# Kernel optimization log

Measured on AMD Instinct MI355X. Metric: run time of the kernel, lower is better.

The kernel has to match this reference:

```python
import jax, jax.numpy as jnp
import numpy as np

B, S, D, H, DFF, L, VOCAB = 4, 2048, 512, 8, 2048, 6, 32000
DK = D // H


def positional_encoding(n_step, d):
    pos = jnp.arange(n_step, dtype=jnp.float32)[:, None]            # (S,1)
    i = jnp.arange(d, dtype=jnp.float32)                            # (D,)
    ang = pos * (1.0 / jnp.power(10000.0, 2.0 * jnp.floor(i / 2.0) / d))
    odd = (jnp.arange(d) % 2).astype(bool)
    return jnp.where(odd, jnp.cos(ang), jnp.sin(ang))               # (S,D)


def layer_norm(x, g, b, eps=1e-6):
    m = x.mean(-1, keepdims=True)
    v = ((x - m) ** 2).mean(-1, keepdims=True)
    return g * (x - m) * jax.lax.rsqrt(v + eps) + b


def mha(Q, K, V, Wq, bq, Wo, bo, mask):
    # Faithful to source: Wq is (buggily) used for Q, K and V projections.
    def split(t):
        return t.reshape(t.shape[0], -1, H, DK).transpose(0, 2, 1, 3)  # (B,H,S,dk)
    q = split(Q @ Wq + bq)
    k = split(K @ Wq + bq)
    v = split(V @ Wq + bq)
    scores = jnp.einsum('bhqd,bhkd->bhqk', q, k) / jnp.sqrt(jnp.float32(DK))
    if mask is not None:
        scores = scores + mask * (-1e9)
    attn = jax.nn.softmax(scores, axis=-1)
    out = jnp.einsum('bhqk,bhkd->bhqd', attn, v)
    out = out.transpose(0, 2, 1, 3).reshape(Q.shape[0], -1, D)
    return out @ Wo + bo


def setup_inputs() -> dict:
    key = jax.random.key(0)
    ks = jax.random.split(key, 16)
    inputs = jax.random.randint(ks[0], (B, S), 0, VOCAB)
    enc_inputs = jax.random.normal(ks[1], (B, S, D), dtype=jnp.float32)
    # causal mask (1 = masked) broadcast over heads, per source mask*-1e9 convention
    comb = 1.0 - jnp.tril(jnp.ones((S, S), dtype=jnp.float32))
    comb_mask = jnp.broadcast_to(comb, (B, 1, S, S))
    padding_mask = jnp.zeros((B, 1, 1, S), dtype=jnp.float32)
    s = 0.02
    emb = jax.random.normal(ks[2], (VOCAB, D), dtype=jnp.float32) * s
    Wq1 = jax.random.normal(ks[3], (L, D, D), dtype=jnp.float32) * s
    bq1 = jnp.zeros((L, D), dtype=jnp.float32)
    Wo1 = jax.random.normal(ks[4], (L, D, D), dtype=jnp.float32) * s
    bo1 = jnp.zeros((L, D), dtype=jnp.float32)
    Wq2 = jax.random.normal(ks[5], (L, D, D), dtype=jnp.float32) * s
    bq2 = jnp.zeros((L, D), dtype=jnp.float32)
    Wo2 = jax.random.normal(ks[6], (L, D, D), dtype=jnp.float32) * s
    bo2 = jnp.zeros((L, D), dtype=jnp.float32)
    W1 = jax.random.normal(ks[7], (L, D, DFF), dtype=jnp.float32) * s
    b1 = jnp.zeros((L, DFF), dtype=jnp.float32)
    W2 = jax.random.normal(ks[8], (L, DFF, D), dtype=jnp.float32) * s
    b2 = jnp.zeros((L, D), dtype=jnp.float32)
    ln_g = jnp.ones((L, 3, D), dtype=jnp.float32)
    ln_b = jnp.zeros((L, 3, D), dtype=jnp.float32)
    return dict(inputs=inputs, enc_inputs=enc_inputs, comb_mask=comb_mask,
                padding_mask=padding_mask, emb=emb, Wq1=Wq1, bq1=bq1, Wo1=Wo1,
                bo1=bo1, Wq2=Wq2, bq2=bq2, Wo2=Wo2, bo2=bo2, W1=W1, b1=b1,
                W2=W2, b2=b2, ln_g=ln_g, ln_b=ln_b)


def reference(inputs, enc_inputs, comb_mask, padding_mask, emb, Wq1, bq1, Wo1,
              bo1, Wq2, bq2, Wo2, bo2, W1, b1, W2, b2, ln_g, ln_b):
    # embedding + sinusoidal positional encoding (dropout = identity at eval)
    x = emb[inputs] * jnp.sqrt(jnp.float32(D)) + positional_encoding(S, D)
    for l in range(L):
        a1 = mha(x, x, x, Wq1[l], bq1[l], Wo1[l], bo1[l], comb_mask)
        x1 = layer_norm(a1 + x, ln_g[l, 0], ln_b[l, 0])
        a2 = mha(x1, enc_inputs, enc_inputs, Wq2[l], bq2[l], Wo2[l], bo2[l], padding_mask)
        x2 = layer_norm(a2 + x1, ln_g[l, 1], ln_b[l, 1])
        f = jax.nn.relu(x2 @ W1[l] + b1[l]) @ W2[l] + b2[l]
        x = layer_norm(x2 + f, ln_g[l, 2], ln_b[l, 2])
    return x
```

## Files before the change

kernel.cpp:

```cpp
#include <hip/hip_runtime.h>
#include <hip/hip_bf16.h>
#include <cstddef>
#include <cstdint>

#define BB   4
#define SS   2048
#define DD   512
#define HH   8
#define DFFC 2048
#define LLC  6
#define DKH  64
#define MMR  (BB * SS)

typedef short s16x8 __attribute__((ext_vector_type(8)));
typedef float f32x4 __attribute__((ext_vector_type(4)));
typedef unsigned short us4 __attribute__((ext_vector_type(4)));
typedef unsigned int u32;

__device__ __forceinline__ unsigned short f2bf(float f) {
  union { float f; unsigned int u; } v; v.f = f;
  const unsigned int u = v.u;
  return (unsigned short)((u + 0x7FFFu + ((u >> 16) & 1u)) >> 16);
}
__device__ __forceinline__ float bflo(u32 u) { return __uint_as_float(u << 16); }
__device__ __forceinline__ float bfhi(u32 u) { return __uint_as_float(u & 0xffff0000u); }

__device__ __forceinline__ s16x8 ld8(const unsigned short* p) {
  return *(const s16x8*)p;
}

__device__ __forceinline__ void gload16(const unsigned short* g, unsigned short* l) {
  __builtin_amdgcn_global_load_lds(
      (const __attribute__((address_space(1))) void*)g,
      (__attribute__((address_space(3))) void*)l, 16, 0, 0);
}

__global__ __launch_bounds__(256) void k_embed_pe(const int* __restrict__ toks,
                                                  const float* __restrict__ emb,
                                                  unsigned short* __restrict__ xb) {
  const int t = blockIdx.x;
  const int s = t & (SS - 1);
  const int tok = toks[t];
  const float ln10k = 9.210340371976184f;
  for (int d = threadIdx.x; d < DD; d += 256) {
    const int e = d >> 1;
    const float ex = 2.0f * (float)e * (1.0f / (float)DD);
    const float freq = expf(-ex * ln10k);
    const float ang = (float)s * freq;
    const float pe = (d & 1) ? cosf(ang) : sinf(ang);
    const float v = emb[(size_t)tok * DD + d] * 22.62741699796952f + pe;
    xb[(size_t)t * DD + d] = f2bf(v);
  }
}

__global__ __launch_bounds__(256) void k_f32_to_bf16(const float* __restrict__ src,
                                                     unsigned short* __restrict__ dst) {
  const int i = (blockIdx.x * 256 + threadIdx.x) * 4;
  const float4 v = *(const float4*)(src + i);
  us4 w;
  w.x = f2bf(v.x); w.y = f2bf(v.y); w.z = f2bf(v.z); w.w = f2bf(v.w);
  *(us4*)(dst + i) = w;
}

__global__ __launch_bounds__(256) void k_wt(const float* s0, const float* s1,
                                            const float* s2, const float* s3,
                                            const float* s4, const float* s5,
                                            unsigned short* d0, unsigned short* d1,
                                            unsigned short* d2, unsigned short* d3,
                                            unsigned short* d4, unsigned short* d5) {
  const int t = blockIdx.x;
  const int tid = threadIdx.x;
  const float* src; unsigned short* dst; int K, N, tile, lntn;
  if (t < 256) {
    const int m = t >> 6; tile = t & 63; K = 512; N = 512; lntn = 3;
    src = (m == 0) ? s0 : (m == 1) ? s1 : (m == 2) ? s2 : s3;
    dst = (m == 0) ? d0 : (m == 1) ? d1 : (m == 2) ? d2 : d3;
  } else if (t < 512) {
    src = s4; dst = d4; K = 512; N = 2048; tile = t - 256; lntn = 5;
  } else {
    src = s5; dst = d5; K = 2048; N = 512; tile = t - 512; lntn = 3;
  }
  const int tn = tile & ((1 << lntn) - 1);
  const int tk = tile >> lntn;
  const int k0 = tk * 64, n0 = tn * 64;

  __shared__ unsigned short T[64][68];
#pragma unroll
  for (int i = 0; i < 4; ++i) {
    const int f = i * 256 + tid;
    const int r = f >> 4, c4 = (f & 15) << 2;
    const float4 v = *(const float4*)(src + (size_t)(k0 + r) * N + n0 + c4);
    us4 w;
    w.x = f2bf(v.x); w.y = f2bf(v.y); w.z = f2bf(v.z); w.w = f2bf(v.w);
    *(us4*)&T[r][c4] = w;
  }
  __syncthreads();
#pragma unroll
  for (int i = 0; i < 4; ++i) {
    const int f = i * 256 + tid;
    const int n = f >> 4, k4 = (f & 15) << 2;
    us4 w;
    w.x = T[k4 + 0][n]; w.y = T[k4 + 1][n];
    w.z = T[k4 + 2][n]; w.w = T[k4 + 3][n];
    *(us4*)&dst[(size_t)(n0 + n) * K + k0 + k4] = w;
  }
}

template<int BN, bool RELU, bool VT>
__global__ __launch_bounds__(256) void k_gemm_mfma(const unsigned short* __restrict__ A,
                                                   const unsigned short* __restrict__ Bt,
                                                   const float* __restrict__ bias,
                                                   unsigned short* __restrict__ Cb,
                                                   unsigned short* __restrict__ Vt,
                                                   int voff, int M, int N, int K) {
  constexpr int NT = BN / 32;
  __shared__ unsigned short As[128 * 64];
  __shared__ unsigned short Bs[BN * 64];

  const int tid = threadIdx.x;
  const int wave = tid >> 6, lane = tid & 63;
  const int quad = lane >> 4, l16 = lane & 15;
  const int wm = wave & 1, wn = wave >> 1;
  const int mbase = blockIdx.x * 128, nbase = blockIdx.y * BN;

  f32x4 acc[4][NT];
#pragma unroll
  for (int mt = 0; mt < 4; ++mt)
#pragma unroll
    for (int nt = 0; nt < NT; ++nt) acc[mt][nt] = (f32x4){0.f, 0.f, 0.f, 0.f};

  for (int kb = 0; kb < K; kb += 64) {
    __syncthreads();
#pragma unroll
    for (int i = 0; i < 4; ++i) {
      const int c = i * 256 + wave * 64 + lane;
      const int m = c >> 3;
      const int k8 = (c & 7) ^ (m & 7);
      gload16(A + (size_t)(mbase + m) * K + kb + k8 * 8,
              As + (size_t)(i * 256 + wave * 64) * 8);
    }
#pragma unroll
    for (int i = 0; i < BN / 32; ++i) {
      const int c = i * 256 + wave * 64 + lane;
      const int n = c >> 3;
      const int k8 = (c & 7) ^ (n & 7);
      gload16(Bt + (size_t)(nbase + n) * K + kb + k8 * 8,
              Bs + (size_t)(i * 256 + wave * 64) * 8);
    }
    __syncthreads();
#pragma unroll
    for (int kh = 0; kh < 2; ++kh) {
      s16x8 af[4];
#pragma unroll
      for (int mt = 0; mt < 4; ++mt) {
        const int m = wm * 64 + mt * 16 + l16;
        const int cc = m * 8 + ((kh * 4 + quad) ^ (m & 7));
        af[mt] = ld8(As + cc * 8);
      }
#pragma unroll
      for (int nt = 0; nt < NT; ++nt) {
        const int n = wn * (BN / 2) + nt * 16 + l16;
        const int cc = n * 8 + ((kh * 4 + quad) ^ (n & 7));
        const s16x8 bf = ld8(Bs + cc * 8);
#pragma unroll
        for (int mt = 0; mt < 4; ++mt)
          acc[mt][nt] = __builtin_amdgcn_mfma_f32_16x16x32_bf16(af[mt], bf, acc[mt][nt], 0, 0, 0);
      }
    }
  }

#pragma unroll
  for (int nt = 0; nt < NT; ++nt) {
    const int col = nbase + wn * (BN / 2) + nt * 16 + l16;
    const float bv = bias[col];
#pragma unroll
    for (int mt = 0; mt < 4; ++mt) {
      const int row0 = mbase + wm * 64 + mt * 16 + quad * 4;
      float vv[4];
#pragma unroll
      for (int r = 0; r < 4; ++r) {
        float v = acc[mt][nt][r] + bv;
        if (RELU) v = fmaxf(v, 0.0f);
        vv[r] = v;
        Cb[(size_t)(row0 + r) * N + col] = f2bf(v);
      }
      if (VT) {
        if (row0 >= voff) {
          const int vrow = row0 - voff;
          const int bb = vrow >> 11, s0 = vrow & 2047;
          us4 o;
          o.x = f2bf(vv[0]); o.y = f2bf(vv[1]); o.z = f2bf(vv[2]); o.w = f2bf(vv[3]);
          *(us4*)(Vt + ((size_t)((bb * 8 + (col >> 6)) * 64 + (col & 63))) * SS + s0) = o;
        }
      }
    }
  }
}

__global__ __launch_bounds__(512) void k_attn_mfma(const unsigned short* __restrict__ Qp,
                                                   const unsigned short* __restrict__ Kp,
                                                   const unsigned short* __restrict__ Vtp,
                                                   unsigned short* __restrict__ Out,
                                                   int causal) {
  __shared__ unsigned short Ks[2][4096];
  __shared__ unsigned short Vs[2][4096];
  __shared__ unsigned short Ps[8][16][72];

  const int hb = blockIdx.x;
  const int h = hb & 7, b = hb >> 3;
  const int by = blockIdx.y;
  const int qt = causal ? ((by < 8) ? (15 - by) : (by - 8)) : by;
  const int tid = threadIdx.x;
  const int w = tid >> 6, lane = tid & 63;
  const int quad = lane >> 4, l16 = lane & 15;

  s16x8 aq[2];
  {
    const int qrow = b * SS + qt * 128 + w * 16 + l16;
#pragma unroll
    for (int kh = 0; kh < 2; ++kh) {
      s16x8 v = *(const s16x8*)(Qp + (size_t)qrow * DD + h * DKH + kh * 32 + quad * 8);
#pragma unroll
      for (int j = 0; j < 8; ++j) {
        const unsigned int u = ((unsigned int)(unsigned short)v[j]) << 16;
        const float f = __uint_as_float(u) * 0.125f;
        v[j] = (short)(unsigned short)(__float_as_uint(f) >> 16);
      }
      aq[kh] = v;
    }
  }

  f32x4 O[4];
  float l_r[4];
#pragma unroll
  for (int i = 0; i < 4; ++i) { O[i] = (f32x4){0.f, 0.f, 0.f, 0.f}; l_r[i] = 0.f; }

  const unsigned short* Kbase = Kp + (size_t)(b * SS) * DD + h * DKH;
  const unsigned short* Vbase = Vtp + (size_t)hb * DKH * SS;

  const int nkt = causal ? (2 * qt + 2) : (SS / 64);

  auto stage = [&](int kt, int buf) {
    const int c = tid;
    const int r = c >> 3, c8 = c & 7;
    gload16(Kbase + (size_t)(kt * 64 + r) * DD + ((c8 ^ (r & 7)) << 3),
            &Ks[buf][(size_t)(w * 64) * 8]);
    gload16(Vbase + (size_t)r * SS + kt * 64 + ((c8 ^ (r & 7)) << 3),
            &Vs[buf][(size_t)(w * 64) * 8]);
  };

  stage(0, 0);
  for (int kt = 0; kt < nkt; ++kt) {
    __syncthreads();
    if (kt + 1 < nkt) stage(kt + 1, (kt + 1) & 1);
    const unsigned short* ks = Ks[kt & 1];
    const unsigned short* vs = Vs[kt & 1];

    f32x4 S[4];
#pragma unroll
    for (int nt = 0; nt < 4; ++nt) {
      const int n = nt * 16 + l16;
      const s16x8 b0 = ld8(ks + (n * 8 + (quad ^ (n & 7))) * 8);
      const s16x8 b1 = ld8(ks + (n * 8 + ((4 + quad) ^ (n & 7))) * 8);
      f32x4 s = (f32x4){0.f, 0.f, 0.f, 0.f};
      s = __builtin_amdgcn_mfma_f32_16x16x32_bf16(aq[0], b0, s, 0, 0, 0);
      s = __builtin_amdgcn_mfma_f32_16x16x32_bf16(aq[1], b1, s, 0, 0, 0);
      S[nt] = s;
    }

    {
      const int qb = qt * 128 + w * 16;
      const bool needmask = causal && (kt * 64 + 63 > qb);
#pragma unroll
      for (int nt = 0; nt < 4; ++nt) {
#pragma unroll
        for (int r = 0; r < 4; ++r) {
          float p = __expf(S[nt][r]);
          if (needmask) {
            const int key = kt * 64 + nt * 16 + l16;
            if (key > qb + quad * 4 + r) p = 0.0f;
          }
          const unsigned int pu = __float_as_uint(p) & 0xffff0000u;
          l_r[r] += __uint_as_float(pu);
          Ps[w][quad * 4 + r][nt * 16 + l16] = (unsigned short)(pu >> 16);
        }
      }
    }
    asm volatile("s_waitcnt lgkmcnt(0)" ::: "memory");

    const s16x8 ap0 = ld8(&Ps[w][l16][quad * 8]);
    const s16x8 ap1 = ld8(&Ps[w][l16][32 + quad * 8]);
#pragma unroll
    for (int nt = 0; nt < 4; ++nt) {
      const int n = nt * 16 + l16;
      const s16x8 b0 = ld8(vs + (n * 8 + (quad ^ (n & 7))) * 8);
      const s16x8 b1 = ld8(vs + (n * 8 + ((4 + quad) ^ (n & 7))) * 8);
      O[nt] = __builtin_amdgcn_mfma_f32_16x16x32_bf16(ap0, b0, O[nt], 0, 0, 0);
      O[nt] = __builtin_amdgcn_mfma_f32_16x16x32_bf16(ap1, b1, O[nt], 0, 0, 0);
    }
  }

  {
    const int qb = qt * 128 + w * 16;
#pragma unroll
    for (int r = 0; r < 4; ++r) {
      float l = l_r[r];
      l += __shfl_xor(l, 1);
      l += __shfl_xor(l, 2);
      l += __shfl_xor(l, 4);
      l += __shfl_xor(l, 8);
      const float linv = 1.0f / l;
      unsigned short* orow = Out + (size_t)(b * SS + qb + quad * 4 + r) * DD + h * DKH;
#pragma unroll
      for (int nt = 0; nt < 4; ++nt)
        orow[nt * 16 + l16] = f2bf(O[nt][r] * linv);
    }
  }
}

__device__ __forceinline__ float block_reduce_sum(float v) {
  __shared__ float red[4];
#pragma unroll
  for (int off = 32; off > 0; off >>= 1) v += __shfl_down(v, off);
  const int lane = threadIdx.x & 63;
  const int w = threadIdx.x >> 6;
  __syncthreads();
  if (lane == 0) red[w] = v;
  __syncthreads();
  return red[0] + red[1] + red[2] + red[3];
}

template<bool F32OUT>
__global__ __launch_bounds__(256) void k_add_ln(const unsigned short* __restrict__ a,
                                                const unsigned short* __restrict__ r,
                                                const float* __restrict__ g,
                                                const float* __restrict__ be,
                                                unsigned short* __restrict__ ob,
                                                float* __restrict__ of) {
  const int row = blockIdx.x;
  const int t = threadIdx.x;
  const size_t base = (size_t)row * DD + t * 2;
  const u32 av = *(const u32*)(a + base);
  const u32 rv = *(const u32*)(r + base);
  const float v0 = bflo(av) + bflo(rv);
  const float v1 = bfhi(av) + bfhi(rv);
  const float s = block_reduce_sum(v0 + v1);
  const float mean = s * (1.0f / (float)DD);
  const float d0 = v0 - mean;
  const float d1 = v1 - mean;
  const float var = block_reduce_sum(d0 * d0 + d1 * d1) * (1.0f / (float)DD);
  const float inv = rsqrtf(var + 1e-6f);
  const float o0 = g[t * 2] * d0 * inv + be[t * 2];
  const float o1 = g[t * 2 + 1] * d1 * inv + be[t * 2 + 1];
  const u32 o = (u32)f2bf(o0) | ((u32)f2bf(o1) << 16);
  *(u32*)(ob + base) = o;
  if (F32OUT) {
    of[base]     = o0;
    of[base + 1] = o1;
  }
}

extern "C" void kernel_launch(void* const* d_in, const int* in_sizes, int n_in,
                              void* d_out, int out_size, void* d_ws, size_t ws_size,
                              hipStream_t stream) {
  const int*   toks = (const int*)d_in[0];
  const float* enc  = (const float*)d_in[1];
  const float* emb  = (const float*)d_in[4];
  const float* Wq1  = (const float*)d_in[5];
  const float* bq1  = (const float*)d_in[6];
  const float* Wo1  = (const float*)d_in[7];
  const float* bo1  = (const float*)d_in[8];
  const float* Wq2  = (const float*)d_in[9];
  const float* bq2  = (const float*)d_in[10];
  const float* Wo2  = (const float*)d_in[11];
  const float* bo2  = (const float*)d_in[12];
  const float* W1   = (const float*)d_in[13];
  const float* b1   = (const float*)d_in[14];
  const float* W2   = (const float*)d_in[15];
  const float* b2   = (const float*)d_in[16];
  const float* lng  = (const float*)d_in[17];
  const float* lnb  = (const float*)d_in[18];
  float* out = (float*)d_out;

  char* p = (char*)d_ws;
  unsigned short* Wq1t = (unsigned short*)p; p += (size_t)512 * 512 * 2;
  unsigned short* Wo1t = (unsigned short*)p; p += (size_t)512 * 512 * 2;
  unsigned short* Wq2t = (unsigned short*)p; p += (size_t)512 * 512 * 2;
  unsigned short* Wo2t = (unsigned short*)p; p += (size_t)512 * 512 * 2;
  unsigned short* W1t  = (unsigned short*)p; p += (size_t)2048 * 512 * 2;
  unsigned short* W2t  = (unsigned short*)p; p += (size_t)512 * 2048 * 2;
  unsigned short* Xcur = (unsigned short*)p; p += (size_t)MMR * DD * 2;
  unsigned short* Cat  = (unsigned short*)p; p += (size_t)2 * MMR * DD * 2;
  unsigned short* Pm   = (unsigned short*)p; p += (size_t)2 * MMR * DD * 2;
  unsigned short* Ab   = (unsigned short*)p; p += (size_t)MMR * DD * 2;
  unsigned short* Gb   = (unsigned short*)p; p += (size_t)MMR * DD * 2;
  unsigned short* X2b  = (unsigned short*)p; p += (size_t)MMR * DD * 2;
  unsigned short* Vt   = (unsigned short*)p; p += (size_t)MMR * DD * 2;
  unsigned short* Hb   = (unsigned short*)p; p += (size_t)MMR * DFFC * 2;
  unsigned short* encb = Cat + (size_t)MMR * DD;

  const dim3 blk(256);
  const dim3 blkA(512);
  const dim3 gP(MMR / 128, DD / 64);
  const dim3 gM(2 * MMR / 128, DD / 64);
  const dim3 gF1(MMR / 128, DFFC / 128);
  const dim3 gAttn(HH * BB, SS / 128);

  k_embed_pe<<<MMR, blk, 0, stream>>>(toks, emb, Xcur);
  k_f32_to_bf16<<<(MMR * DD) / 1024, blk, 0, stream>>>(enc, encb);

  for (int l = 0; l < LLC; ++l) {
    const float* wq1 = Wq1 + (size_t)l * DD * DD;
    const float* wo1 = Wo1 + (size_t)l * DD * DD;
    const float* wq2 = Wq2 + (size_t)l * DD * DD;
    const float* wo2 = Wo2 + (size_t)l * DD * DD;
    const float* w1  = W1  + (size_t)l * DD * DFFC;
    const float* w2  = W2  + (size_t)l * DFFC * DD;
    const float* bq1l = bq1 + (size_t)l * DD;
    const float* bo1l = bo1 + (size_t)l * DD;
    const float* bq2l = bq2 + (size_t)l * DD;
    const float* bo2l = bo2 + (size_t)l * DD;
    const float* b1l  = b1  + (size_t)l * DFFC;
    const float* b2l  = b2  + (size_t)l * DD;
    const float* g0 = lng + ((size_t)l * 3 + 0) * DD;
    const float* e0 = lnb + ((size_t)l * 3 + 0) * DD;
    const float* g1 = lng + ((size_t)l * 3 + 1) * DD;
    const float* e1 = lnb + ((size_t)l * 3 + 1) * DD;
    const float* g2 = lng + ((size_t)l * 3 + 2) * DD;
    const float* e2 = lnb + ((size_t)l * 3 + 2) * DD;

    k_wt<<<768, blk, 0, stream>>>(wq1, wo1, wq2, wo2, w1, w2,
                                  Wq1t, Wo1t, Wq2t, Wo2t, W1t, W2t);

    k_gemm_mfma<64, false, true><<<gP, blk, 0, stream>>>(Xcur, Wq1t, bq1l, Pm, Vt, 0, MMR, DD, DD);
    k_attn_mfma<<<gAttn, blkA, 0, stream>>>(Pm, Pm, Vt, Ab, 1);
    k_gemm_mfma<64, false, false><<<gP, blk, 0, stream>>>(Ab, Wo1t, bo1l, Gb, nullptr, 0, MMR, DD, DD);
    k_add_ln<false><<<MMR, blk, 0, stream>>>(Gb, Xcur, g0, e0, Cat, nullptr);

    k_gemm_mfma<64, false, true><<<gM, blk, 0, stream>>>(Cat, Wq2t, bq2l, Pm, Vt, MMR, 2 * MMR, DD, DD);
    k_attn_mfma<<<gAttn, blkA, 0, stream>>>(Pm, Pm + (size_t)MMR * DD, Vt, Ab, 0);
    k_gemm_mfma<64, false, false><<<gP, blk, 0, stream>>>(Ab, Wo2t, bo2l, Gb, nullptr, 0, MMR, DD, DD);
    k_add_ln<false><<<MMR, blk, 0, stream>>>(Gb, Cat, g1, e1, X2b, nullptr);

    k_gemm_mfma<128, true, false><<<gF1, blk, 0, stream>>>(X2b, W1t, b1l, Hb, nullptr, 0, MMR, DFFC, DD);
    k_gemm_mfma<64, false, false><<<gP, blk, 0, stream>>>(Hb, W2t, b2l, Gb, nullptr, 0, MMR, DD, DFFC);
    if (l == LLC - 1)
      k_add_ln<true><<<MMR, blk, 0, stream>>>(Gb, X2b, g2, e2, Xcur, out);
    else
      k_add_ln<false><<<MMR, blk, 0, stream>>>(Gb, X2b, g2, e2, Xcur, nullptr);
  }
}
```

Baseline: 1.670 ms.

## Load attention K/V fragments directly from global into registers, drop LDS staging

The attention kernel no longer stages K and Vt tiles into shared memory and no longer synchronises the block on each tile. Each wave loads its MFMA operand fragments straight from global memory into registers, prefetching the next K tile and loading V after computing scores. Launch bounds now request 4 blocks per CU. The aim is to remove barrier and LDS round-trip costs. In exchange, each of the 8 waves reads the same K/V data redundantly from global/L2, and the register pressure is higher.

```diff
diff --git a/kernel.cpp b/kernel.cpp
--- a/kernel.cpp
+++ b/kernel.cpp
@@ -197,13 +197,11 @@
   }
 }
 
-__global__ __launch_bounds__(512) void k_attn_mfma(const unsigned short* __restrict__ Qp,
-                                                   const unsigned short* __restrict__ Kp,
-                                                   const unsigned short* __restrict__ Vtp,
-                                                   unsigned short* __restrict__ Out,
-                                                   int causal) {
-  __shared__ unsigned short Ks[2][4096];
-  __shared__ unsigned short Vs[2][4096];
+__global__ __launch_bounds__(512, 4) void k_attn_mfma(const unsigned short* __restrict__ Qp,
+                                                      const unsigned short* __restrict__ Kp,
+                                                      const unsigned short* __restrict__ Vtp,
+                                                      unsigned short* __restrict__ Out,
+                                                      int causal) {
   __shared__ unsigned short Ps[8][16][72];
 
   const int hb = blockIdx.x;
@@ -235,38 +233,41 @@
 #pragma unroll
   for (int i = 0; i < 4; ++i) { O[i] = (f32x4){0.f, 0.f, 0.f, 0.f}; l_r[i] = 0.f; }
 
-  const unsigned short* Kbase = Kp + (size_t)(b * SS) * DD + h * DKH;
-  const unsigned short* Vbase = Vtp + (size_t)hb * DKH * SS;
+  const unsigned short* Kb = Kp + (size_t)(b * SS) * DD + h * DKH;
+  const unsigned short* Vb = Vtp + (size_t)hb * DKH * SS;
 
   const int nkt = causal ? (2 * qt + 2) : (SS / 64);
 
-  auto stage = [&](int kt, int buf) {
-    const int c = tid;
-    const int r = c >> 3, c8 = c & 7;
-    gload16(Kbase + (size_t)(kt * 64 + r) * DD + ((c8 ^ (r & 7)) << 3),
-            &Ks[buf][(size_t)(w * 64) * 8]);
-    gload16(Vbase + (size_t)r * SS + kt * 64 + ((c8 ^ (r & 7)) << 3),
-            &Vs[buf][(size_t)(w * 64) * 8]);
-  };
-
-  stage(0, 0);
+  s16x8 kf[8];
+#pragma unroll
+  for (int nt = 0; nt < 4; ++nt)
+#pragma unroll
+    for (int kh = 0; kh < 2; ++kh)
+      kf[nt * 2 + kh] = ld8(Kb + (size_t)(nt * 16 + l16) * DD + kh * 32 + quad * 8);
+
   for (int kt = 0; kt < nkt; ++kt) {
-    __syncthreads();
-    if (kt + 1 < nkt) stage(kt + 1, (kt + 1) & 1);
-    const unsigned short* ks = Ks[kt & 1];
-    const unsigned short* vs = Vs[kt & 1];
-
     f32x4 S[4];
 #pragma unroll
     for (int nt = 0; nt < 4; ++nt) {
-      const int n = nt * 16 + l16;
-      const s16x8 b0 = ld8(ks + (n * 8 + (quad ^ (n & 7))) * 8);
-      const s16x8 b1 = ld8(ks + (n * 8 + ((4 + quad) ^ (n & 7))) * 8);
       f32x4 s = (f32x4){0.f, 0.f, 0.f, 0.f};
-      s = __builtin_amdgcn_mfma_f32_16x16x32_bf16(aq[0], b0, s, 0, 0, 0);
-      s = __builtin_amdgcn_mfma_f32_16x16x32_bf16(aq[1], b1, s, 0, 0, 0);
+      s = __builtin_amdgcn_mfma_f32_16x16x32_bf16(aq[0], kf[nt * 2 + 0], s, 0, 0, 0);
+      s = __builtin_amdgcn_mfma_f32_16x16x32_bf16(aq[1], kf[nt * 2 + 1], s, 0, 0, 0);
       S[nt] = s;
     }
+
+    s16x8 vf[8];
+#pragma unroll
+    for (int nt = 0; nt < 4; ++nt)
+#pragma unroll
+      for (int kh = 0; kh < 2; ++kh)
+        vf[nt * 2 + kh] = ld8(Vb + (size_t)(nt * 16 + l16) * SS + kt * 64 + kh * 32 + quad * 8);
+
+    const int ktn = (kt + 1 < nkt) ? (kt + 1) : kt;
+#pragma unroll
+    for (int nt = 0; nt < 4; ++nt)
+#pragma unroll
+      for (int kh = 0; kh < 2; ++kh)
+        kf[nt * 2 + kh] = ld8(Kb + (size_t)(ktn * 64 + nt * 16 + l16) * DD + kh * 32 + quad * 8);
 
     {
       const int qb = qt * 128 + w * 16;
@@ -292,11 +293,8 @@
     const s16x8 ap1 = ld8(&Ps[w][l16][32 + quad * 8]);
 #pragma unroll
     for (int nt = 0; nt < 4; ++nt) {
-      const int n = nt * 16 + l16;
-      const s16x8 b0 = ld8(vs + (n * 8 + (quad ^ (n & 7))) * 8);
-      const s16x8 b1 = ld8(vs + (n * 8 + ((4 + quad) ^ (n & 7))) * 8);
-      O[nt] = __builtin_amdgcn_mfma_f32_16x16x32_bf16(ap0, b0, O[nt], 0, 0, 0);
-      O[nt] = __builtin_amdgcn_mfma_f32_16x16x32_bf16(ap1, b1, O[nt], 0, 0, 0);
+      O[nt] = __builtin_amdgcn_mfma_f32_16x16x32_bf16(ap0, vf[nt * 2 + 0], O[nt], 0, 0, 0);
+      O[nt] = __builtin_amdgcn_mfma_f32_16x16x32_bf16(ap1, vf[nt * 2 + 1], O[nt], 0, 0, 0);
     }
   }
 
```

Result: slower. 3.132 ms (+87.5%).
